# Kernel tuning notes

Measured on AMD Instinct MI355X. Metric: run time of the kernel, lower is better.

## Reference

```python
import jax, jax.numpy as jnp
import numpy as np

B, T, I, H = 64, 2048, 512, 512


def setup_inputs() -> dict:
    key = jax.random.key(0)
    ks = jax.random.split(key, 17)
    def xav(k, shape):
        fan_in, fan_out = shape
        lim = np.sqrt(6.0 / (fan_in + fan_out)).astype(np.float32)
        return jax.random.uniform(k, shape, jnp.float32, -lim, lim)
    inp = {"x": jax.random.normal(ks[0], (B, T, I), jnp.float32)}
    names = ["i", "f", "g", "o"]
    for n, g in enumerate(names):
        inp[f"w_i{g}"] = xav(ks[1 + 4 * n], (I, H))
        inp[f"w_h{g}"] = xav(ks[2 + 4 * n], (H, H))
        inp[f"b_i{g}"] = jnp.zeros((H,), jnp.float32)
        inp[f"b_h{g}"] = jnp.zeros((H,), jnp.float32)
    return inp


def reference(x, w_ii, w_hi, b_ii, b_hi, w_if, w_hf, b_if, b_hf,
              w_ig, w_hg, b_ig, b_hg, w_io, w_ho, b_io, b_ho):
    batch = x.shape[0]
    h0 = jnp.zeros((batch, w_hi.shape[0]), x.dtype)
    c0 = jnp.zeros((batch, w_hi.shape[0]), x.dtype)

    def step(carry, x_t):
        h, c = carry
        i_t = jax.nn.sigmoid(x_t @ w_ii + b_ii + h @ w_hi + b_hi)
        f_t = jax.nn.sigmoid(x_t @ w_if + b_if + h @ w_hf + b_hf)
        g_t = jnp.tanh(x_t @ w_ig + b_ig + h @ w_hg + b_hg)
        o_t = jax.nn.sigmoid(x_t @ w_io + b_io + h @ w_ho + b_ho)
        c_new = f_t * c + i_t * g_t
        h_new = o_t * jnp.tanh(c_new)
        return (h_new, c_new), None

    # scan over time: x -> (T, B, I)
    (h_t, c_t), _ = jax.lax.scan(step, (h0, c0), jnp.swapaxes(x, 0, 1))
    return (h_t, c_t)
```

## Files before the change

kernel.cpp:

```cpp
#include <hip/hip_runtime.h>


typedef __attribute__((ext_vector_type(8))) short bf16x8;
typedef __attribute__((ext_vector_type(4))) float f32x4;

#define T_STEPS 2048

__device__ __forceinline__ unsigned short f2bf(float f) {
  union { float f; unsigned u; } v; v.f = f;
  unsigned r = v.u + 0x7fffu + ((v.u >> 16) & 1u);
  return (unsigned short)(r >> 16);
}
__device__ __forceinline__ float bf2f(unsigned short b) {
  union { unsigned u; float f; } v; v.u = ((unsigned)b) << 16;
  return v.f;
}
__device__ __forceinline__ float sigm(float x)  { return 1.f / (1.f + __expf(-x)); }
__device__ __forceinline__ float tanhx(float x) { return 2.f / (1.f + __expf(-2.f * x)) - 1.f; }

__global__ __launch_bounds__(256) void k_cvt(const float* __restrict__ x,
                                             unsigned short* __restrict__ xb, int n4) {
  int stride = gridDim.x * blockDim.x;
  for (int i = blockIdx.x * blockDim.x + threadIdx.x; i < n4; i += stride) {
    float4 v = ((const float4*)x)[i];
    ushort4 o;
    o.x = f2bf(v.x); o.y = f2bf(v.y); o.z = f2bf(v.z); o.w = f2bf(v.w);
    ((ushort4*)xb)[i] = o;
  }
}

__global__ __launch_bounds__(128) void k_prep_w(
    const float* __restrict__ wi, const float* __restrict__ wf,
    const float* __restrict__ wg, const float* __restrict__ wo,
    const float* __restrict__ bii, const float* __restrict__ bif,
    const float* __restrict__ big, const float* __restrict__ bio,
    const float* __restrict__ bhi, const float* __restrict__ bhf,
    const float* __restrict__ bhg, const float* __restrict__ bho,
    unsigned short* __restrict__ Wt, float* __restrict__ biasp) {
  int p = blockIdx.x;
  int g = (p >> 4) & 3, jj = p >> 6, hl = p & 15;
  int hcol = jj * 16 + hl;
  const float* w = (g == 0) ? wi : (g == 1) ? wf : (g == 2) ? wg : wo;
  for (int k = threadIdx.x; k < 512; k += 128)
    Wt[(long)p * 512 + k] = f2bf(w[(long)k * 512 + hcol]);
  if (threadIdx.x == 0) {
    const float* bi = (g == 0) ? bii : (g == 1) ? bif : (g == 2) ? big : bio;
    const float* bh = (g == 0) ? bhi : (g == 1) ? bhf : (g == 2) ? bhg : bho;
    biasp[p] = bi[hcol] + bh[hcol];
  }
}

__global__ __launch_bounds__(256) void k_gemm_x(
    const unsigned short* __restrict__ A,
    const unsigned short* __restrict__ Bt,
    const float* __restrict__ biasp,
    unsigned short* __restrict__ Gx) {
  __shared__ unsigned short lds[16384];
  unsigned short* lA = lds;
  unsigned short* lB = lds + 8192;
  const int tid  = threadIdx.x;
  const int lane = tid & 63;
  const int wave = tid >> 6;
  const long m0  = (long)blockIdx.x * 128;
  const int p0   = blockIdx.y * 128;
  const int wm   = (wave >> 1) * 64;
  const int wn   = (wave & 1) * 64;
  const int lrow = lane & 15;
  const int quad = lane >> 4;

  f32x4 acc[4][4] = {};

  for (int kb = 0; kb < 512; kb += 64) {
    __syncthreads();
#pragma unroll
    for (int it = 0; it < 4; ++it) {
      int ci = it * 256 + tid;
      int row = ci >> 3, c8 = ci & 7;
      int c8p = c8 ^ (row & 7);
      *(int4*)&lA[row * 64 + c8p * 8] = *(const int4*)(A + (m0 + row) * 512 + kb + c8 * 8);
      *(int4*)&lB[row * 64 + c8p * 8] = *(const int4*)(Bt + (long)(p0 + row) * 512 + kb + c8 * 8);
    }
    __syncthreads();
#pragma unroll
    for (int kk = 0; kk < 2; ++kk) {
      int c8 = kk * 4 + quad;
      bf16x8 af[4], bfr[4];
#pragma unroll
      for (int i = 0; i < 4; ++i) {
        int m = wm + i * 16 + lrow;
        af[i]  = *(const bf16x8*)&lA[m * 64 + ((c8 ^ (m & 7)) * 8)];
        int p = wn + i * 16 + lrow;
        bfr[i] = *(const bf16x8*)&lB[p * 64 + ((c8 ^ (p & 7)) * 8)];
      }
#pragma unroll
      for (int i = 0; i < 4; ++i)
#pragma unroll
        for (int n = 0; n < 4; ++n)
          acc[i][n] = __builtin_amdgcn_mfma_f32_16x16x32_bf16(af[i], bfr[n], acc[i][n], 0, 0, 0);
    }
  }

  float bl[4];
#pragma unroll
  for (int n = 0; n < 4; ++n) bl[n] = biasp[p0 + wn + n * 16 + lrow];

  __syncthreads();
#pragma unroll
  for (int i = 0; i < 4; ++i)
#pragma unroll
    for (int n = 0; n < 4; ++n) {
      int col = wn + n * 16 + lrow;
#pragma unroll
      for (int r4 = 0; r4 < 4; ++r4) {
        int row = wm + i * 16 + quad * 4 + r4;
        lds[row * 128 + col] = f2bf(acc[i][n][r4] + bl[n]);
      }
    }
  __syncthreads();
  {
    int row = tid >> 1, half = tid & 1;
    long m = m0 + row;
    int b = (int)(m >> 11), t = (int)(m & 2047);
    int bg = b >> 4, r = b & 15;
    int jj = (p0 >> 6) + half;
    unsigned short* dst = Gx + ((((long)t * 32 + jj) * 4 + bg) * 16 + r) * 64;
    const unsigned short* src = lds + row * 128 + half * 64;
#pragma unroll
    for (int c = 0; c < 8; ++c)
      *(int4*)(dst + c * 8) = *(const int4*)(src + c * 8);
  }
}

__global__ __launch_bounds__(512, 1) void k_lstm(
    const float* __restrict__ Whi, const float* __restrict__ Whf,
    const float* __restrict__ Whg, const float* __restrict__ Who,
    const unsigned short* __restrict__ Gx,
    unsigned long long* __restrict__ hbuf,
    float* __restrict__ out) {
  const int wg   = blockIdx.x;
  const int bg   = wg >> 4;
  const int slot = wg & 15;
  const int tid  = threadIdx.x;
  const int lane = tid & 63;
  const int wave = tid >> 6;
  const int gate = wave & 3;
  const int kh   = wave >> 2;
  const int hl   = lane & 15;
  const int quad = lane >> 4;
  const int j0   = slot * 32;

  __shared__ float gl[4][2][16][33];
  __shared__ alignas(1024) unsigned char hlds[16 * 1024];

  const float* Wh = (gate == 0) ? Whi : (gate == 1) ? Whf : (gate == 2) ? Whg : Who;
  union WFrag { bf16x8 v; unsigned u[4]; };
  WFrag wfrag[2][8];
#pragma unroll
  for (int cs = 0; cs < 2; ++cs) {
    const int hcol = j0 + cs * 16 + hl;
#pragma unroll
    for (int kk = 0; kk < 8; ++kk) {
      int kbase = kh * 256 + kk * 32 + quad * 8;
      bf16x8 t;
#pragma unroll
      for (int i = 0; i < 8; ++i)
        t[i] = (short)f2bf(Wh[(long)(kbase + i) * 512 + hcol]);
      wfrag[cs][kk].v = t;
    }
  }
#pragma unroll
  for (int cs = 0; cs < 2; ++cs)
#pragma unroll
    for (int kk = 0; kk < 8; ++kk)
#pragma unroll
      for (int r = 0; r < 4; ++r)
        asm volatile("" : "+v"(wfrag[cs][kk].u[r]));

  unsigned long long* hb0 = hbuf;
  unsigned long long* hb1 = hbuf + 64 * 256;

  const int er  = tid >> 5;
  const int ec  = tid & 31;
  const int r_a = lane & 15;

  float c_val = 0.f;
  float h_val = 0.f;

  for (int s = 0; s < T_STEPS; ++s) {
    const unsigned short* gxp =
        Gx + ((((long)s * 32 + (j0 >> 4) + (ec >> 4)) * 4 + bg) * 16 + er) * 64 + (ec & 15);
    unsigned short gxi = gxp[0], gxf = gxp[16], gxg = gxp[32], gxo = gxp[48];

    const unsigned long long* hcur = (s & 1) ? hb1 : hb0;
    unsigned long long* hnxt       = (s & 1) ? hb0 : hb1;
    const unsigned long long* hbase = hcur + bg * 4096;
    const unsigned exp_tag = (unsigned)s;

    unsigned long long w[8];
#pragma unroll
    for (int c = 0; c < 8; ++c)
      w[c] = __hip_atomic_load(hbase + c * 512 + tid, __ATOMIC_RELAXED,
                               __HIP_MEMORY_SCOPE_AGENT);
    for (;;) {
      unsigned miss = 0;
#pragma unroll
      for (int c = 0; c < 8; ++c)
        miss |= ((((unsigned)(w[c] >> 32)) != exp_tag) ? 1u : 0u) << c;
      if (!__any((int)(miss != 0))) break;
#pragma unroll
      for (int c = 0; c < 8; ++c)
        if (miss & (1u << c))
          w[c] = __hip_atomic_load(hbase + c * 512 + tid, __ATOMIC_RELAXED,
                                   __HIP_MEMORY_SCOPE_AGENT);
    }

#pragma unroll
    for (int c = 0; c < 8; ++c) {
      int wv  = c * 512 + tid;
      int row = wv >> 8, cp = wv & 255;
      *(unsigned*)(hlds + row * 1024 + ((cp * 4) ^ ((row & 7) << 4))) = (unsigned)w[c];
    }
    __syncthreads();

    f32x4 acc0 = {0.f, 0.f, 0.f, 0.f};
    f32x4 acc1 = {0.f, 0.f, 0.f, 0.f};
#pragma unroll
    for (int kk = 0; kk < 8; ++kk) {
      int b0 = kh * 512 + kk * 64 + quad * 16;
      bf16x8 af = *(const bf16x8*)(hlds + r_a * 1024 + (b0 ^ ((r_a & 7) << 4)));
      acc0 = __builtin_amdgcn_mfma_f32_16x16x32_bf16(af, wfrag[0][kk].v, acc0, 0, 0, 0);
      acc1 = __builtin_amdgcn_mfma_f32_16x16x32_bf16(af, wfrag[1][kk].v, acc1, 0, 0, 0);
    }
#pragma unroll
    for (int i = 0; i < 4; ++i) {
      gl[gate][kh][quad * 4 + i][hl]      = acc0[i];
      gl[gate][kh][quad * 4 + i][16 + hl] = acc1[i];
    }
    __syncthreads();

    float ui = gl[0][0][er][ec] + gl[0][1][er][ec] + bf2f(gxi);
    float uf = gl[1][0][er][ec] + gl[1][1][er][ec] + bf2f(gxf);
    float ug = gl[2][0][er][ec] + gl[2][1][er][ec] + bf2f(gxg);
    float uo = gl[3][0][er][ec] + gl[3][1][er][ec] + bf2f(gxo);
    float ig = sigm(ui), fg = sigm(uf), gg = tanhx(ug), og = sigm(uo);
    c_val = fg * c_val + ig * gg;
    h_val = og * tanhx(c_val);

    unsigned hv = (unsigned)f2bf(h_val);
    unsigned other = (unsigned)__shfl_xor((int)hv, 1, 64);
    if (!(tid & 1)) {
      unsigned pack = (hv & 0xffffu) | (other << 16);
      unsigned long long word =
          (((unsigned long long)(unsigned)(s + 1)) << 32) | (unsigned long long)pack;
      int cp = (j0 + ec) >> 1;
      __hip_atomic_store(hnxt + (bg * 16 + er) * 256 + cp, word,
                         __ATOMIC_RELAXED, __HIP_MEMORY_SCOPE_AGENT);
    }
    __syncthreads();
  }

  int b = bg * 16 + er;
  out[(long)b * 512 + j0 + ec]         = h_val;
  out[32768 + (long)b * 512 + j0 + ec] = c_val;
}

extern "C" void kernel_launch(void* const* d_in, const int* in_sizes, int n_in,
                              void* d_out, int out_size, void* d_ws, size_t ws_size,
                              hipStream_t stream) {
  const float* x    = (const float*)d_in[0];
  const float* w_ii = (const float*)d_in[1];
  const float* w_hi = (const float*)d_in[2];
  const float* b_ii = (const float*)d_in[3];
  const float* b_hi = (const float*)d_in[4];
  const float* w_if = (const float*)d_in[5];
  const float* w_hf = (const float*)d_in[6];
  const float* b_if_= (const float*)d_in[7];
  const float* b_hf = (const float*)d_in[8];
  const float* w_ig = (const float*)d_in[9];
  const float* w_hg = (const float*)d_in[10];
  const float* b_ig = (const float*)d_in[11];
  const float* b_hg = (const float*)d_in[12];
  const float* w_io = (const float*)d_in[13];
  const float* w_ho = (const float*)d_in[14];
  const float* b_io = (const float*)d_in[15];
  const float* b_ho = (const float*)d_in[16];

  char* ws = (char*)d_ws;
  unsigned short* Gx   = (unsigned short*)(ws);
  unsigned short* xb   = (unsigned short*)(ws + 536870912L);
  unsigned short* Wt   = (unsigned short*)(ws + 671088640L);
  float* biasp         = (float*)(ws + 673185792L);
  unsigned long long* hbuf = (unsigned long long*)(ws + 673193984L);

  hipMemsetAsync(hbuf, 0, 2L * 64 * 256 * 8, stream);

  k_cvt<<<8192, 256, 0, stream>>>(x, xb, (64 * 2048 * 512) / 4);
  k_prep_w<<<2048, 128, 0, stream>>>(w_ii, w_if, w_ig, w_io,
                                     b_ii, b_if_, b_ig, b_io,
                                     b_hi, b_hf, b_hg, b_ho,
                                     Wt, biasp);
  k_gemm_x<<<dim3(1024, 16), 256, 0, stream>>>(xb, Wt, biasp, Gx);
  k_lstm<<<64, 512, 0, stream>>>(w_hi, w_hf, w_hg, w_ho, Gx, hbuf, (float*)d_out);
}
```

Baseline: 5.544 ms.

## Fuse input GEMM and LSTM recurrence into one kernel with per-chunk readiness counters

Merges the input-projection GEMM and the recurrent LSTM kernel into a single launch. The first 64 blocks run the recurrence and the remaining blocks compute Gx tiles ordered by 128-timestep chunks, each bumping a per-chunk atomic counter. The recurrent blocks spin on that counter before starting each chunk, so the recurrence can begin while later Gx chunks are still being produced. The change also splits the recurrent MFMA chain into two independent accumulators and drops the trailing per-step barrier. It relies on the 64 recurrent blocks being scheduled before or alongside the GEMM blocks, otherwise it could deadlock, and the 512-thread GEMM tiles with one block per CU may lower GEMM efficiency.

```diff
diff --git a/kernel.cpp b/kernel.cpp
--- a/kernel.cpp
+++ b/kernel.cpp
@@ -50,107 +50,116 @@
   }
 }
 
-__global__ __launch_bounds__(256) void k_gemm_x(
+__global__ __launch_bounds__(512, 1) void k_fused(
+    const float* __restrict__ Whi, const float* __restrict__ Whf,
+    const float* __restrict__ Whg, const float* __restrict__ Who,
+    unsigned short* __restrict__ Gx,
+    unsigned long long* __restrict__ hbuf,
+    unsigned int* __restrict__ tcnt,
+    float* __restrict__ out,
     const unsigned short* __restrict__ A,
     const unsigned short* __restrict__ Bt,
-    const float* __restrict__ biasp,
-    unsigned short* __restrict__ Gx) {
-  __shared__ unsigned short lds[16384];
-  unsigned short* lA = lds;
-  unsigned short* lB = lds + 8192;
+    const float* __restrict__ biasp) {
+  __shared__ __align__(1024) unsigned char smem[33792];
   const int tid  = threadIdx.x;
   const int lane = tid & 63;
   const int wave = tid >> 6;
-  const long m0  = (long)blockIdx.x * 128;
-  const int p0   = blockIdx.y * 128;
-  const int wm   = (wave >> 1) * 64;
-  const int wn   = (wave & 1) * 64;
-  const int lrow = lane & 15;
   const int quad = lane >> 4;
 
-  f32x4 acc[4][4] = {};
-
-  for (int kb = 0; kb < 512; kb += 64) {
-    __syncthreads();
-#pragma unroll
-    for (int it = 0; it < 4; ++it) {
-      int ci = it * 256 + tid;
-      int row = ci >> 3, c8 = ci & 7;
-      int c8p = c8 ^ (row & 7);
-      *(int4*)&lA[row * 64 + c8p * 8] = *(const int4*)(A + (m0 + row) * 512 + kb + c8 * 8);
-      *(int4*)&lB[row * 64 + c8p * 8] = *(const int4*)(Bt + (long)(p0 + row) * 512 + kb + c8 * 8);
-    }
-    __syncthreads();
-#pragma unroll
-    for (int kk = 0; kk < 2; ++kk) {
-      int c8 = kk * 4 + quad;
-      bf16x8 af[4], bfr[4];
-#pragma unroll
-      for (int i = 0; i < 4; ++i) {
-        int m = wm + i * 16 + lrow;
-        af[i]  = *(const bf16x8*)&lA[m * 64 + ((c8 ^ (m & 7)) * 8)];
-        int p = wn + i * 16 + lrow;
-        bfr[i] = *(const bf16x8*)&lB[p * 64 + ((c8 ^ (p & 7)) * 8)];
+  if (blockIdx.x >= 64) {
+    unsigned short* lA = (unsigned short*)smem;
+    unsigned short* lB = lA + 8192;
+    unsigned short* lC = (unsigned short*)smem;
+    const int tileid = blockIdx.x - 64;
+    const int t128   = tileid >> 10;
+    const int rem    = tileid & 1023;
+    const long m0    = (long)(rem >> 4) * 2048 + t128 * 128;
+    const int p0     = (rem & 15) * 128;
+    const int wm     = (wave >> 2) * 64;
+    const int wn     = (wave & 3) * 32;
+    const int lrow   = lane & 15;
+
+    f32x4 acc[4][2] = {};
+
+    for (int kb = 0; kb < 512; kb += 64) {
+      __syncthreads();
+#pragma unroll
+      for (int it = 0; it < 2; ++it) {
+        int ci = it * 512 + tid;
+        int row = ci >> 3, c8 = ci & 7;
+        int c8p = c8 ^ (row & 7);
+        *(int4*)&lA[row * 64 + c8p * 8] = *(const int4*)(A + (m0 + row) * 512 + kb + c8 * 8);
+        *(int4*)&lB[row * 64 + c8p * 8] = *(const int4*)(Bt + (long)(p0 + row) * 512 + kb + c8 * 8);
       }
-#pragma unroll
-      for (int i = 0; i < 4; ++i)
-#pragma unroll
-        for (int n = 0; n < 4; ++n)
-          acc[i][n] = __builtin_amdgcn_mfma_f32_16x16x32_bf16(af[i], bfr[n], acc[i][n], 0, 0, 0);
-    }
-  }
-
-  float bl[4];
-#pragma unroll
-  for (int n = 0; n < 4; ++n) bl[n] = biasp[p0 + wn + n * 16 + lrow];
-
-  __syncthreads();
-#pragma unroll
-  for (int i = 0; i < 4; ++i)
-#pragma unroll
-    for (int n = 0; n < 4; ++n) {
-      int col = wn + n * 16 + lrow;
-#pragma unroll
-      for (int r4 = 0; r4 < 4; ++r4) {
-        int row = wm + i * 16 + quad * 4 + r4;
-        lds[row * 128 + col] = f2bf(acc[i][n][r4] + bl[n]);
+      __syncthreads();
+#pragma unroll
+      for (int kk = 0; kk < 2; ++kk) {
+        int c8 = kk * 4 + quad;
+        bf16x8 af[4], bfr[2];
+#pragma unroll
+        for (int i = 0; i < 4; ++i) {
+          int m = wm + i * 16 + lrow;
+          af[i]  = *(const bf16x8*)&lA[m * 64 + ((c8 ^ (m & 7)) * 8)];
+        }
+#pragma unroll
+        for (int n = 0; n < 2; ++n) {
+          int p = wn + n * 16 + lrow;
+          bfr[n] = *(const bf16x8*)&lB[p * 64 + ((c8 ^ (p & 7)) * 8)];
+        }
+#pragma unroll
+        for (int i = 0; i < 4; ++i)
+#pragma unroll
+          for (int n = 0; n < 2; ++n)
+            acc[i][n] = __builtin_amdgcn_mfma_f32_16x16x32_bf16(af[i], bfr[n], acc[i][n], 0, 0, 0);
       }
     }
-  __syncthreads();
-  {
-    int row = tid >> 1, half = tid & 1;
-    long m = m0 + row;
-    int b = (int)(m >> 11), t = (int)(m & 2047);
-    int bg = b >> 4, r = b & 15;
-    int jj = (p0 >> 6) + half;
-    unsigned short* dst = Gx + ((((long)t * 32 + jj) * 4 + bg) * 16 + r) * 64;
-    const unsigned short* src = lds + row * 128 + half * 64;
-#pragma unroll
-    for (int c = 0; c < 8; ++c)
-      *(int4*)(dst + c * 8) = *(const int4*)(src + c * 8);
-  }
-}
-
-__global__ __launch_bounds__(512, 1) void k_lstm(
-    const float* __restrict__ Whi, const float* __restrict__ Whf,
-    const float* __restrict__ Whg, const float* __restrict__ Who,
-    const unsigned short* __restrict__ Gx,
-    unsigned long long* __restrict__ hbuf,
-    float* __restrict__ out) {
+
+    float bl[2];
+#pragma unroll
+    for (int n = 0; n < 2; ++n) bl[n] = biasp[p0 + wn + n * 16 + lrow];
+
+    __syncthreads();
+#pragma unroll
+    for (int i = 0; i < 4; ++i)
+#pragma unroll
+      for (int n = 0; n < 2; ++n) {
+        int col = wn + n * 16 + lrow;
+#pragma unroll
+        for (int r4 = 0; r4 < 4; ++r4) {
+          int row = wm + i * 16 + quad * 4 + r4;
+          lC[row * 128 + col] = f2bf(acc[i][n][r4] + bl[n]);
+        }
+      }
+    __syncthreads();
+    {
+      int row = tid >> 2, seg = tid & 3;
+      long m = m0 + row;
+      int b = (int)(m >> 11), t = (int)(m & 2047);
+      int bg = b >> 4, r = b & 15;
+      int jj = (p0 >> 6) + (seg >> 1);
+      unsigned short* dst = Gx + ((((long)t * 32 + jj) * 4 + bg) * 16 + r) * 64 + (seg & 1) * 32;
+      const unsigned short* src = lC + row * 128 + seg * 32;
+#pragma unroll
+      for (int c = 0; c < 4; ++c)
+        *(int4*)(dst + c * 8) = *(const int4*)(src + c * 8);
+    }
+    asm volatile("s_waitcnt vmcnt(0)" ::: "memory");
+    __syncthreads();
+    if (tid == 0)
+      __hip_atomic_fetch_add(&tcnt[t128], 1u, __ATOMIC_RELEASE, __HIP_MEMORY_SCOPE_AGENT);
+    return;
+  }
+
+  float (*gl)[2][16][33] = (float (*)[2][16][33])smem;
+  unsigned char* hlds = smem + 17408;
+
   const int wg   = blockIdx.x;
   const int bg   = wg >> 4;
   const int slot = wg & 15;
-  const int tid  = threadIdx.x;
-  const int lane = tid & 63;
-  const int wave = tid >> 6;
   const int gate = wave & 3;
   const int kh   = wave >> 2;
   const int hl   = lane & 15;
-  const int quad = lane >> 4;
   const int j0   = slot * 32;
-
-  __shared__ float gl[4][2][16][33];
-  __shared__ alignas(1024) unsigned char hlds[16 * 1024];
 
   const float* Wh = (gate == 0) ? Whi : (gate == 1) ? Whf : (gate == 2) ? Whg : Who;
   union WFrag { bf16x8 v; unsigned u[4]; };
@@ -187,6 +196,15 @@
   float h_val = 0.f;
 
   for (int s = 0; s < T_STEPS; ++s) {
+    if ((s & 127) == 0) {
+      if (tid == 0) {
+        while (__hip_atomic_load(&tcnt[s >> 7], __ATOMIC_ACQUIRE,
+                                 __HIP_MEMORY_SCOPE_AGENT) < 1024u)
+          __builtin_amdgcn_s_sleep(8);
+      }
+      __syncthreads();
+    }
+
     const unsigned short* gxp =
         Gx + ((((long)s * 32 + (j0 >> 4) + (ec >> 4)) * 4 + bg) * 16 + er) * 64 + (ec & 15);
     unsigned short gxi = gxp[0], gxf = gxp[16], gxg = gxp[32], gxo = gxp[48];
@@ -222,15 +240,19 @@
     }
     __syncthreads();
 
-    f32x4 acc0 = {0.f, 0.f, 0.f, 0.f};
-    f32x4 acc1 = {0.f, 0.f, 0.f, 0.f};
-#pragma unroll
-    for (int kk = 0; kk < 8; ++kk) {
+    f32x4 a0e = {0.f,0.f,0.f,0.f}, a0o = {0.f,0.f,0.f,0.f};
+    f32x4 a1e = {0.f,0.f,0.f,0.f}, a1o = {0.f,0.f,0.f,0.f};
+#pragma unroll
+    for (int kk = 0; kk < 8; kk += 2) {
       int b0 = kh * 512 + kk * 64 + quad * 16;
-      bf16x8 af = *(const bf16x8*)(hlds + r_a * 1024 + (b0 ^ ((r_a & 7) << 4)));
-      acc0 = __builtin_amdgcn_mfma_f32_16x16x32_bf16(af, wfrag[0][kk].v, acc0, 0, 0, 0);
-      acc1 = __builtin_amdgcn_mfma_f32_16x16x32_bf16(af, wfrag[1][kk].v, acc1, 0, 0, 0);
-    }
+      bf16x8 afe = *(const bf16x8*)(hlds + r_a * 1024 + (b0 ^ ((r_a & 7) << 4)));
+      bf16x8 afo = *(const bf16x8*)(hlds + r_a * 1024 + ((b0 + 64) ^ ((r_a & 7) << 4)));
+      a0e = __builtin_amdgcn_mfma_f32_16x16x32_bf16(afe, wfrag[0][kk].v,     a0e, 0, 0, 0);
+      a1e = __builtin_amdgcn_mfma_f32_16x16x32_bf16(afe, wfrag[1][kk].v,     a1e, 0, 0, 0);
+      a0o = __builtin_amdgcn_mfma_f32_16x16x32_bf16(afo, wfrag[0][kk + 1].v, a0o, 0, 0, 0);
+      a1o = __builtin_amdgcn_mfma_f32_16x16x32_bf16(afo, wfrag[1][kk + 1].v, a1o, 0, 0, 0);
+    }
+    f32x4 acc0 = a0e + a0o, acc1 = a1e + a1o;
 #pragma unroll
     for (int i = 0; i < 4; ++i) {
       gl[gate][kh][quad * 4 + i][hl]      = acc0[i];
@@ -256,7 +278,6 @@
       __hip_atomic_store(hnxt + (bg * 16 + er) * 256 + cp, word,
                          __ATOMIC_RELAXED, __HIP_MEMORY_SCOPE_AGENT);
     }
-    __syncthreads();
   }
 
   int b = bg * 16 + er;
@@ -291,14 +312,16 @@
   unsigned short* Wt   = (unsigned short*)(ws + 671088640L);
   float* biasp         = (float*)(ws + 673185792L);
   unsigned long long* hbuf = (unsigned long long*)(ws + 673193984L);
-
-  hipMemsetAsync(hbuf, 0, 2L * 64 * 256 * 8, stream);
+  unsigned int* tcnt   = (unsigned int*)(ws + 673193984L + 2L * 64 * 256 * 8);
+
+  hipMemsetAsync(hbuf, 0, 2L * 64 * 256 * 8 + 64, stream);
 
   k_cvt<<<8192, 256, 0, stream>>>(x, xb, (64 * 2048 * 512) / 4);
   k_prep_w<<<2048, 128, 0, stream>>>(w_ii, w_if, w_ig, w_io,
                                      b_ii, b_if_, b_ig, b_io,
                                      b_hi, b_hf, b_hg, b_ho,
                                      Wt, biasp);
-  k_gemm_x<<<dim3(1024, 16), 256, 0, stream>>>(xb, Wt, biasp, Gx);
-  k_lstm<<<64, 512, 0, stream>>>(w_hi, w_hf, w_hg, w_ho, Gx, hbuf, (float*)d_out);
-}
+  k_fused<<<64 + 16384, 512, 0, stream>>>(w_hi, w_hf, w_hg, w_ho,
+                                          Gx, hbuf, tcnt, (float*)d_out,
+                                          xb, Wt, biasp);
+}
```

Measured after the change: 7.100 ms. 28.1% more time.
